# Performance work log

Measured on AMD Instinct MI355X. Metric: run time of the kernel, lower is better.

Reference implementation:

```python
import jax, jax.numpy as jnp
import numpy as np

D_MODEL = 1024
N_HEADS = 16
HEAD_DIM = D_MODEL // N_HEADS


def setup_inputs() -> dict:
    key = jax.random.key(0)
    k_x, k_wqkv, k_bqkv, k_wo, k_bo = jax.random.split(key, 5)
    lim_qkv = 1.0 / np.sqrt(D_MODEL)
    return {
        "x": jax.random.normal(k_x, (2, 4096, D_MODEL), dtype=jnp.float32),
        "w_qkv": jax.random.uniform(k_wqkv, (D_MODEL, 3 * D_MODEL), minval=-lim_qkv, maxval=lim_qkv, dtype=jnp.float32),
        "b_qkv": jax.random.uniform(k_bqkv, (3 * D_MODEL,), minval=-lim_qkv, maxval=lim_qkv, dtype=jnp.float32),
        "w_out": jax.random.uniform(k_wo, (D_MODEL, D_MODEL), minval=-lim_qkv, maxval=lim_qkv, dtype=jnp.float32),
        "b_out": jax.random.uniform(k_bo, (D_MODEL,), minval=-lim_qkv, maxval=lim_qkv, dtype=jnp.float32),
    }


def reference(x, w_qkv, b_qkv, w_out, b_out):
    b, s, _ = x.shape
    scale = HEAD_DIM ** -0.5
    qkv = x @ w_qkv + b_qkv                              # [b, s, 3*d]
    qkv = qkv.reshape(b, s, 3, N_HEADS, HEAD_DIM)
    qkv = jnp.transpose(qkv, (2, 0, 3, 1, 4))            # [3, b, h, s, hd]
    q, k, v = qkv[0], qkv[1], qkv[2]
    scores = jnp.einsum("bhqd,bhkd->bhqk", q, k) * scale  # [b, h, s, s]
    causal = jnp.triu(jnp.ones((s, s), dtype=bool), k=1)
    scores = jnp.where(causal, -jnp.inf, scores)
    probs = jax.nn.softmax(scores, axis=-1)
    out = jnp.einsum("bhqk,bhkd->bhqd", probs, v)         # [b, h, s, hd]
    out = jnp.transpose(out, (0, 2, 1, 3)).reshape(b, s, D_MODEL)
    return out @ w_out + b_out
```

## Files before the change

### kernel.cpp

```cpp
#include <hip/hip_runtime.h>
#include <math.h>

#define S_LEN 4096
#define DM    1024
#define NHEAD 16
#define HDIM  64
#define C3    3072
#define CL2E  0.180336880f

typedef __attribute__((ext_vector_type(8))) short bf8_t;
typedef __attribute__((ext_vector_type(4))) float f32x4;
typedef __attribute__((ext_vector_type(16))) float f32x16;

__device__ __forceinline__ short f2bf(float f) {
    union { float f; unsigned u; } v; v.f = f;
    unsigned r = v.u + 0x7FFF + ((v.u >> 16) & 1);
    return (short)(r >> 16);
}
__device__ __forceinline__ float fexp2(float x) { return __builtin_amdgcn_exp2f(x); }

__device__ __forceinline__ unsigned cvtpk(float a, float b) {
    unsigned r;
    asm("v_cvt_pk_bf16_f32 %0, %1, %2" : "=v"(r) : "v"(a), "v"(b));
    return r;
}

__device__ __forceinline__ void gload_lds16(const void* g, void* l) {
    __builtin_amdgcn_global_load_lds(
        (const __attribute__((address_space(1))) unsigned int*)g,
        (__attribute__((address_space(3))) unsigned int*)l, 16, 0, 0);
}

__device__ __forceinline__ float vsum16(f32x16 s) {
    float a = (s[0] + s[1]) + (s[2] + s[3]);
    float b = (s[4] + s[5]) + (s[6] + s[7]);
    float c = (s[8] + s[9]) + (s[10] + s[11]);
    float d = (s[12] + s[13]) + (s[14] + s[15]);
    return (a + b) + (c + d);
}

__global__ void cast_f32_bf16(const float* __restrict__ in, short* __restrict__ out, int n8)
{
    int i = blockIdx.x * blockDim.x + threadIdx.x;
    if (i < n8) {
        float4 a = ((const float4*)in)[i * 2];
        float4 b = ((const float4*)in)[i * 2 + 1];
        bf8_t v = {f2bf(a.x), f2bf(a.y), f2bf(a.z), f2bf(a.w),
                   f2bf(b.x), f2bf(b.y), f2bf(b.z), f2bf(b.w)};
        ((bf8_t*)out)[i] = v;
    }
}

__global__ __launch_bounds__(256)
void transpose_cast(const float* __restrict__ in, short* __restrict__ out, int R, int C)
{
    __shared__ float t[32][33];
    const int tx = threadIdx.x & 31;
    const int ty = threadIdx.x >> 5;
    const int r0 = blockIdx.y * 32;
    const int c0 = blockIdx.x * 32;
    #pragma unroll
    for (int i = 0; i < 32; i += 8)
        t[ty + i][tx] = in[(size_t)(r0 + ty + i) * C + c0 + tx];
    __syncthreads();
    #pragma unroll
    for (int i = 0; i < 32; i += 8)
        out[(size_t)(c0 + ty + i) * R + r0 + tx] = f2bf(t[tx][ty + i]);
}

__global__ __launch_bounds__(256)
void transpose_v(const short* __restrict__ qkv, short* __restrict__ vt)
{
    __shared__ short t[64][72];
    const int st = blockIdx.x, bh = blockIdx.y;
    const int b = bh >> 4, h = bh & 15;
    const int tid = threadIdx.x;
    const int r   = tid >> 2;
    const int c16 = (tid & 3) * 16;
    const short* src = qkv + (size_t)b * S_LEN * C3 + 2 * DM + h * HDIM;
    const short* sp  = src + (size_t)(st * 64 + r) * C3 + c16;
    *(bf8_t*)&t[r][c16]     = *(const bf8_t*)sp;
    *(bf8_t*)&t[r][c16 + 8] = *(const bf8_t*)(sp + 8);
    __syncthreads();
    short tmp[16];
    #pragma unroll
    for (int i = 0; i < 16; ++i) tmp[i] = t[c16 + i][r];
    short* dp = vt + (size_t)bh * HDIM * S_LEN + (size_t)r * S_LEN + st * 64 + c16;
    *(bf8_t*)dp       = *(bf8_t*)&tmp[0];
    *(bf8_t*)(dp + 8) = *(bf8_t*)&tmp[8];
}

template<bool BF16OUT, bool QSCALE>
__global__ __launch_bounds__(256)
void gemm_mfma(const short* __restrict__ A, const short* __restrict__ Bt,
               const float* __restrict__ bias, void* __restrict__ Cout,
               int M, int N)
{
    constexpr int K = 1024;
    __shared__ __align__(16) short As[128 * 64];
    __shared__ __align__(16) short Bs[128 * 64];

    const int nbx = N / 128;
    const int nwg = (M / 128) * nbx;
    int bid = blockIdx.x;
    bid = (bid & 7) * (nwg >> 3) + (bid >> 3);
    const int by = bid / nbx, bx = bid % nbx;
    const int row0 = by * 128, col0 = bx * 128;

    const int tid  = threadIdx.x;
    const int lane = tid & 63;
    const int w    = tid >> 6;
    const int l15  = lane & 15;
    const int l4   = lane >> 4;
    const int wr   = w >> 1, wc = w & 1;

    f32x4 acc[4][4];
    #pragma unroll
    for (int i = 0; i < 4; ++i)
        #pragma unroll
        for (int j = 0; j < 4; ++j) acc[i][j] = (f32x4){0.f, 0.f, 0.f, 0.f};

    size_t goff[4];
    int    loff[4];
    #pragma unroll
    for (int i = 0; i < 4; ++i) {
        const int o   = (w * 4 + i) * 1024 + lane * 16;
        const int row = o >> 7;
        const int col = (o & 127) ^ ((row & 7) << 4);
        goff[i] = (size_t)row * (K * 2) + col;
        loff[i] = o;
    }
    const char* Ab = (const char*)A  + (size_t)row0 * (K * 2);
    const char* Bb = (const char*)Bt + (size_t)col0 * (K * 2);

    for (int k0 = 0; k0 < K; k0 += 64) {
        __syncthreads();
        #pragma unroll
        for (int i = 0; i < 4; ++i) {
            gload_lds16(Ab + goff[i] + k0 * 2, (char*)As + loff[i]);
            gload_lds16(Bb + goff[i] + k0 * 2, (char*)Bs + loff[i]);
        }
        __syncthreads();

        #pragma unroll
        for (int ks = 0; ks < 2; ++ks) {
            bf8_t af[4], bfr[4];
            #pragma unroll
            for (int mi = 0; mi < 4; ++mi) {
                const int row = wr * 64 + mi * 16 + l15;
                const int off = (row * 128 + ks * 64 + l4 * 16) ^ ((row & 7) << 4);
                af[mi] = *(bf8_t*)((char*)As + off);
            }
            #pragma unroll
            for (int ni = 0; ni < 4; ++ni) {
                const int row = wc * 64 + ni * 16 + l15;
                const int off = (row * 128 + ks * 64 + l4 * 16) ^ ((row & 7) << 4);
                bfr[ni] = *(bf8_t*)((char*)Bs + off);
            }
            #pragma unroll
            for (int mi = 0; mi < 4; ++mi)
                #pragma unroll
                for (int ni = 0; ni < 4; ++ni)
                    acc[mi][ni] = __builtin_amdgcn_mfma_f32_16x16x32_bf16(
                        af[mi], bfr[ni], acc[mi][ni], 0, 0, 0);
        }
    }

    const float cscale = (QSCALE && col0 < 1024) ? CL2E : 1.0f;

    float bv[4];
    #pragma unroll
    for (int ni = 0; ni < 4; ++ni)
        bv[ni] = bias[col0 + wc * 64 + ni * 16 + l15];

    #pragma unroll
    for (int mi = 0; mi < 4; ++mi)
        #pragma unroll
        for (int r = 0; r < 4; ++r) {
            const int row = row0 + wr * 64 + mi * 16 + l4 * 4 + r;
            #pragma unroll
            for (int ni = 0; ni < 4; ++ni) {
                const int col = col0 + wc * 64 + ni * 16 + l15;
                const float val = (acc[mi][ni][r] + bv[ni]) * cscale;
                if constexpr (BF16OUT)
                    ((short*)Cout)[(size_t)row * N + col] = f2bf(val);
                else
                    ((float*)Cout)[(size_t)row * N + col] = val;
            }
        }
}

__global__ __launch_bounds__(256)
void attn_mfma32(const short* __restrict__ qkv, const short* __restrict__ vt,
                 short* __restrict__ out)
{
    const int lin = blockIdx.x + 16 * blockIdx.y;
    const int xcd = lin & 7;
    const int idx = lin >> 3;
    const int bh  = xcd * 4 + (idx >> 4);
    const int g   = idx & 15;

    const int b   = bh >> 4, h = bh & 15;
    const int tid = threadIdx.x;
    const int lane = tid & 63;
    const int w    = tid >> 6;
    const int l31  = lane & 31;
    const int hi   = lane >> 5;

    __shared__ __align__(16) short lds[2][2][64 * 64];

    const float NEG = -1e30f;

    const short* qkb = qkv + (size_t)b * S_LEN * C3 + h * HDIM;

    const int sr = tid >> 3;
    const int sc = ((tid & 7) * 16) ^ ((sr & 7) << 4);
    const char* srcK = (const char*)(qkb + DM) + (size_t)sr * (C3 * 2) + sc;
    const char* srcV = (const char*)(vt + (size_t)bh * HDIM * S_LEN)
                       + (size_t)sr * (S_LEN * 2) + sc;
    const int ldst = tid * 16;

    #pragma unroll 1
    for (int half = 0; half < 2; ++half) {
        const int qb     = half ? g : (31 - g);
        const int Q0     = qb * 128;
        const int nkt    = qb * 2 + 2;
        const int qmin_w = Q0 + w * 32;
        const int qmax_w = qmin_w + 31;
        const int q_g    = qmin_w + l31;
        const int nkt_w  = (qmax_w >> 6) + 1;

        bf8_t qf[4];
        {
            const short* qp = qkb + (size_t)q_g * C3 + hi * 8;
            qf[0] = *(const bf8_t*)(qp);
            qf[1] = *(const bf8_t*)(qp + 16);
            qf[2] = *(const bf8_t*)(qp + 32);
            qf[3] = *(const bf8_t*)(qp + 48);
        }

        f32x16 o0, o1;
        #pragma unroll
        for (int r = 0; r < 16; ++r) { o0[r] = 0.f; o1[r] = 0.f; }
        float l = 0.f;

        gload_lds16(srcK,                     (char*)lds + ldst);
        gload_lds16(srcK + 32 * (C3 * 2),     (char*)lds + 4096 + ldst);
        gload_lds16(srcV,                     (char*)lds + 8192 + ldst);
        gload_lds16(srcV + 32 * (S_LEN * 2),  (char*)lds + 12288 + ldst);
        __syncthreads();

        for (int kt = 0; kt < nkt; ++kt) {
            const int cur = kt & 1;
            if (kt + 1 < nkt) {
                const char* sK = srcK + (size_t)(kt + 1) * 64 * (C3 * 2);
                const char* sV = srcV + (size_t)(kt + 1) * 64 * 2;
                char* dstb = (char*)lds + (cur ^ 1) * 16384;
                gload_lds16(sK,                    dstb + ldst);
                gload_lds16(sK + 32 * (C3 * 2),    dstb + 4096 + ldst);
                gload_lds16(sV,                    dstb + 8192 + ldst);
                gload_lds16(sV + 32 * (S_LEN * 2), dstb + 12288 + ldst);
            }

            if (kt < nkt_w) {
                const char* Kb = (char*)lds + cur * 16384;
                const char* Vb = Kb + 8192;
                const int kb0 = kt * 64;
                const bool act1 = (kb0 + 32) <= qmax_w;

                f32x16 s0, s1;
                #pragma unroll
                for (int r = 0; r < 16; ++r) { s0[r] = 0.f; s1[r] = NEG; }
                __builtin_amdgcn_s_setprio(1);
                #pragma unroll
                for (int ds = 0; ds < 4; ++ds) {
                    const int R0 = l31;
                    const int off0 = (R0 * 128 + ds * 32 + hi * 16) ^ ((R0 & 7) << 4);
                    bf8_t kf = *(const bf8_t*)(Kb + off0);
                    s0 = __builtin_amdgcn_mfma_f32_32x32x16_bf16(kf, qf[ds], s0, 0, 0, 0);
                }
                if (act1) {
                    #pragma unroll
                    for (int r = 0; r < 16; ++r) s1[r] = 0.f;
                    #pragma unroll
                    for (int ds = 0; ds < 4; ++ds) {
                        const int R1 = 32 + l31;
                        const int off1 = (R1 * 128 + ds * 32 + hi * 16) ^ ((R1 & 7) << 4);
                        bf8_t kf = *(const bf8_t*)(Kb + off1);
                        s1 = __builtin_amdgcn_mfma_f32_32x32x16_bf16(kf, qf[ds], s1, 0, 0, 0);
                    }
                }
                __builtin_amdgcn_s_setprio(0);

                if (kb0 + 31 > qmin_w) {
                    #pragma unroll
                    for (int r = 0; r < 16; ++r) {
                        const int k = kb0 + 4 * hi + ((r & 3) + 8 * (r >> 2));
                        if (k > q_g) s0[r] = NEG;
                    }
                }
                if (act1 && (kb0 + 63 > qmin_w)) {
                    #pragma unroll
                    for (int r = 0; r < 16; ++r) {
                        const int k = kb0 + 32 + 4 * hi + ((r & 3) + 8 * (r >> 2));
                        if (k > q_g) s1[r] = NEG;
                    }
                }

                #pragma unroll
                for (int r = 0; r < 16; ++r) s0[r] = fexp2(s0[r]);
                #pragma unroll
                for (int r = 0; r < 16; ++r) s1[r] = fexp2(s1[r]);

                l += vsum16(s0) + vsum16(s1);

                unsigned W0[2][4], W1[2][4];
                #pragma unroll
                for (int gg = 0; gg < 4; ++gg) {
                    W0[0][gg] = cvtpk(s0[4 * gg], s0[4 * gg + 1]);
                    W1[0][gg] = cvtpk(s0[4 * gg + 2], s0[4 * gg + 3]);
                    W0[1][gg] = cvtpk(s1[4 * gg], s1[4 * gg + 1]);
                    W1[1][gg] = cvtpk(s1[4 * gg + 2], s1[4 * gg + 3]);
                }

                #pragma unroll
                for (int c = 0; c < 4; ++c) {
                    const int t  = c >> 1;
                    const int gA = 2 * (c & 1);
                    const int gB = gA + 1;
                    const unsigned rx0 = __shfl_xor(hi ? W0[t][gA] : W0[t][gB], 32);
                    const unsigned rx1 = __shfl_xor(hi ? W1[t][gA] : W1[t][gB], 32);
                    union { unsigned u[4]; bf8_t v; } pf;
                    pf.u[0] = hi ? rx0 : W0[t][gA];
                    pf.u[1] = hi ? rx1 : W1[t][gA];
                    pf.u[2] = hi ? W0[t][gB] : rx0;
                    pf.u[3] = hi ? W1[t][gB] : rx1;

                    __builtin_amdgcn_s_setprio(1);
                    {
                        const int R = l31;
                        const int off = (R * 128 + c * 32 + hi * 16) ^ ((R & 7) << 4);
                        bf8_t vf = *(const bf8_t*)(Vb + off);
                        o0 = __builtin_amdgcn_mfma_f32_32x32x16_bf16(pf.v, vf, o0, 0, 0, 0);
                    }
                    {
                        const int R = 32 + l31;
                        const int off = (R * 128 + c * 32 + hi * 16) ^ ((R & 7) << 4);
                        bf8_t vf = *(const bf8_t*)(Vb + off);
                        o1 = __builtin_amdgcn_mfma_f32_32x32x16_bf16(pf.v, vf, o1, 0, 0, 0);
                    }
                    __builtin_amdgcn_s_setprio(0);
                }
            }
            __syncthreads();
        }

        const float lt = l + __shfl_xor(l, 32);
        const float inv = 1.f / lt;
        #pragma unroll
        for (int r = 0; r < 16; ++r) {
            const int cr = 4 * hi + ((r & 3) + 8 * (r >> 2));
            const float iv = __shfl(inv, cr);
            const int row = Q0 + w * 32 + cr;
            short* op = out + (size_t)(b * S_LEN + row) * DM + h * HDIM + l31;
            op[0]  = f2bf(o0[r] * iv);
            op[32] = f2bf(o1[r] * iv);
        }
    }
}

extern "C" void kernel_launch(void* const* d_in, const int* in_sizes, int n_in,
                              void* d_out, int out_size, void* d_ws, size_t ws_size,
                              hipStream_t stream)
{
    const float* x     = (const float*)d_in[0];
    const float* w_qkv = (const float*)d_in[1];
    const float* b_qkv = (const float*)d_in[2];
    const float* w_out = (const float*)d_in[3];
    const float* b_out = (const float*)d_in[4];
    float* out = (float*)d_out;

    const int M = 2 * S_LEN;

    char* ws = (char*)d_ws;
    short* qkvb  = (short*)(ws);
    short* attnb = (short*)(ws + 50331648);
    short* xb    = (short*)(ws + 67108864);
    short* wqkvT = (short*)(ws + 83886080);
    short* woutT = (short*)(ws + 90177536);
    short* vtb   = (short*)(ws + 92274688);

    cast_f32_bf16<<<dim3((M * DM / 8 + 255) / 256), 256, 0, stream>>>(x, xb, M * DM / 8);
    transpose_cast<<<dim3(C3 / 32, DM / 32), 256, 0, stream>>>(w_qkv, wqkvT, DM, C3);
    transpose_cast<<<dim3(DM / 32, DM / 32), 256, 0, stream>>>(w_out, woutT, DM, DM);

    gemm_mfma<true, true><<<dim3((M / 128) * (C3 / 128)), 256, 0, stream>>>(
        xb, wqkvT, b_qkv, qkvb, M, C3);

    transpose_v<<<dim3(S_LEN / 64, 2 * NHEAD), 256, 0, stream>>>(qkvb, vtb);

    attn_mfma32<<<dim3(16, 2 * NHEAD), 256, 0, stream>>>(qkvb, vtb, attnb);

    gemm_mfma<false, false><<<dim3((M / 128) * (DM / 128)), 256, 0, stream>>>(
        attnb, woutT, b_out, out, M, DM);
}
```

Baseline: 217.5 us.

## Split attention blocks into two-wave halves to double block count

Each attention block previously ran four waves covering 128 query rows. It now runs two waves covering 64 query rows, and the grid is doubled to 1024 blocks. The block holding the lower waves stops one key tile earlier, which trims causal work that was wasted. The intent is better occupancy and load balance across CUs. The cost is that K/V tiles are loaded twice as often in total, and the staging loop now issues four 16-row copies per tensor to suit 128 threads.

```diff
diff --git a/kernel.cpp b/kernel.cpp
--- a/kernel.cpp
+++ b/kernel.cpp
@@ -190,20 +190,22 @@
         }
 }
 
-__global__ __launch_bounds__(256)
+__global__ __launch_bounds__(128)
 void attn_mfma32(const short* __restrict__ qkv, const short* __restrict__ vt,
                  short* __restrict__ out)
 {
-    const int lin = blockIdx.x + 16 * blockIdx.y;
-    const int xcd = lin & 7;
-    const int idx = lin >> 3;
-    const int bh  = xcd * 4 + (idx >> 4);
-    const int g   = idx & 15;
+    const int lin  = blockIdx.x + 32 * blockIdx.y;
+    const int xcd  = lin & 7;
+    const int idx  = lin >> 3;
+    const int bh   = xcd * 4 + (idx >> 5);
+    const int rem  = idx & 31;
+    const int g    = rem >> 1;
+    const int wb   = (rem & 1) * 2;
 
     const int b   = bh >> 4, h = bh & 15;
     const int tid = threadIdx.x;
     const int lane = tid & 63;
-    const int w    = tid >> 6;
+    const int w    = wb + (tid >> 6);
     const int l31  = lane & 31;
     const int hi   = lane >> 5;
 
@@ -224,7 +226,7 @@
     for (int half = 0; half < 2; ++half) {
         const int qb     = half ? g : (31 - g);
         const int Q0     = qb * 128;
-        const int nkt    = qb * 2 + 2;
+        const int nkt    = qb * 2 + 1 + (wb >> 1);
         const int qmin_w = Q0 + w * 32;
         const int qmax_w = qmin_w + 31;
         const int q_g    = qmin_w + l31;
@@ -244,10 +246,13 @@
         for (int r = 0; r < 16; ++r) { o0[r] = 0.f; o1[r] = 0.f; }
         float l = 0.f;
 
-        gload_lds16(srcK,                     (char*)lds + ldst);
-        gload_lds16(srcK + 32 * (C3 * 2),     (char*)lds + 4096 + ldst);
-        gload_lds16(srcV,                     (char*)lds + 8192 + ldst);
-        gload_lds16(srcV + 32 * (S_LEN * 2),  (char*)lds + 12288 + ldst);
+        #pragma unroll
+        for (int p = 0; p < 4; ++p) {
+            gload_lds16(srcK + (size_t)p * 16 * (C3 * 2),
+                        (char*)lds + p * 2048 + ldst);
+            gload_lds16(srcV + (size_t)p * 16 * (S_LEN * 2),
+                        (char*)lds + 8192 + p * 2048 + ldst);
+        }
         __syncthreads();
 
         for (int kt = 0; kt < nkt; ++kt) {
@@ -256,10 +261,13 @@
                 const char* sK = srcK + (size_t)(kt + 1) * 64 * (C3 * 2);
                 const char* sV = srcV + (size_t)(kt + 1) * 64 * 2;
                 char* dstb = (char*)lds + (cur ^ 1) * 16384;
-                gload_lds16(sK,                    dstb + ldst);
-                gload_lds16(sK + 32 * (C3 * 2),    dstb + 4096 + ldst);
-                gload_lds16(sV,                    dstb + 8192 + ldst);
-                gload_lds16(sV + 32 * (S_LEN * 2), dstb + 12288 + ldst);
+                #pragma unroll
+                for (int p = 0; p < 4; ++p) {
+                    gload_lds16(sK + (size_t)p * 16 * (C3 * 2),
+                                dstb + p * 2048 + ldst);
+                    gload_lds16(sV + (size_t)p * 16 * (S_LEN * 2),
+                                dstb + 8192 + p * 2048 + ldst);
+                }
             }
 
             if (kt < nkt_w) {
@@ -399,7 +407,7 @@
 
     transpose_v<<<dim3(S_LEN / 64, 2 * NHEAD), 256, 0, stream>>>(qkvb, vtb);
 
-    attn_mfma32<<<dim3(16, 2 * NHEAD), 256, 0, stream>>>(qkvb, vtb, attnb);
+    attn_mfma32<<<dim3(32, 2 * NHEAD), 128, 0, stream>>>(qkvb, vtb, attnb);
 
     gemm_mfma<false, false><<<dim3((M / 128) * (DM / 128)), 256, 0, stream>>>(
         attnb, woutT, b_out, out, M, DM);
```

Result: slower. 227.5 us (+4.6%).
